# Kernel optimization log

Measured on AMD Instinct MI355X. Metric: run time of the kernel, lower is better.

## Reference

```python
import jax, jax.numpy as jnp
import numpy as np

N, M, E = 100000, 500, 300000
XS, GS, OUT, HEADS = 100, 100, 100, 2
SLOPE = 0.2
EPS = 1e-12


def l2norm(x, axis):
    n = jnp.linalg.norm(x, axis=axis, keepdims=True)
    return x / jnp.maximum(n, EPS)


def gat_layer(h_ijk, ends, n, W, att):
    # W: [heads*out, in_dim] (no bias); att: [1, heads, out]
    heads, out = att.shape[1], att.shape[2]
    c = (h_ijk @ W.T).reshape(-1, heads, out)               # [E, H, D]
    a = jnp.sum(att * c, axis=2, keepdims=True)             # [E, H, 1]
    e = jnp.exp(-jax.nn.leaky_relu(a, SLOPE))
    denom = jax.ops.segment_sum(e, ends, num_segments=n)    # [n, H, 1]
    alpha = e / denom[ends]                                 # segment softmax (dropout=eval/identity)
    h = jax.ops.segment_sum(alpha * c, ends, num_segments=n)  # [n, H, D]
    h = jax.nn.elu(h)
    h = l2norm(h, axis=2)
    return h.reshape(n, heads * out)


def merge_layer(h_in, h_out, Wi, bi, Wo, bo, Wl, bl):
    hi = h_in @ Wi.T + bi
    ho = h_out @ Wo.T + bo
    lam = jax.nn.sigmoid(jnp.concatenate([hi, ho], axis=1) @ Wl.T + bl)
    h = lam * hi + (1.0 - lam) * ho
    return l2norm(jax.nn.elu(h), axis=1)


def setup_inputs() -> dict:
    key = jax.random.key(0)
    ks = jax.random.split(key, 24)
    D = HEADS * OUT  # 200
    in1 = 2 * XS + GS   # 300
    in2 = 3 * D         # 600
    s = 0.05
    return {
        'edge_idx': jax.random.randint(ks[0], (2, E), 0, N),
        'edge_type': jax.random.randint(ks[1], (E,), 0, M),
        'path_idx': jax.random.randint(ks[2], (2, 8), 0, N),
        'path_type': jax.random.randint(ks[3], (2, 8), 0, M),
        'use_path': 0,
        'x': jax.random.normal(ks[4], (N, XS), jnp.float32),
        'g': jax.random.normal(ks[5], (M, GS), jnp.float32),
        'W_in1': s * jax.random.normal(ks[6], (D, in1), jnp.float32),
        'att_in1': s * jax.random.normal(ks[7], (1, HEADS, OUT), jnp.float32),
        'W_out1': s * jax.random.normal(ks[8], (D, in1), jnp.float32),
        'att_out1': s * jax.random.normal(ks[9], (1, HEADS, OUT), jnp.float32),
        'Wi1': s * jax.random.normal(ks[10], (D, D), jnp.float32), 'bi1': jnp.zeros((D,), jnp.float32),
        'Wo1': s * jax.random.normal(ks[11], (D, D), jnp.float32), 'bo1': jnp.zeros((D,), jnp.float32),
        'Wl1': s * jax.random.normal(ks[12], (1, 2 * D), jnp.float32), 'bl1': jnp.zeros((1,), jnp.float32),
        'Wr': s * jax.random.normal(ks[13], (D, GS), jnp.float32), 'br': jnp.zeros((D,), jnp.float32),
        'Wf': s * jax.random.normal(ks[14], (D, in1), jnp.float32), 'bf': jnp.zeros((D,), jnp.float32),
        'W_in2': s * jax.random.normal(ks[15], (D, in2), jnp.float32),
        'att_in2': s * jax.random.normal(ks[16], (1, 1, D), jnp.float32),
        'W_out2': s * jax.random.normal(ks[17], (D, in2), jnp.float32),
        'att_out2': s * jax.random.normal(ks[18], (1, 1, D), jnp.float32),
        'Wi2': s * jax.random.normal(ks[19], (D, D), jnp.float32), 'bi2': jnp.zeros((D,), jnp.float32),
        'Wo2': s * jax.random.normal(ks[20], (D, D), jnp.float32), 'bo2': jnp.zeros((D,), jnp.float32),
        'Wl2': s * jax.random.normal(ks[21], (1, 2 * D), jnp.float32), 'bl2': jnp.zeros((1,), jnp.float32),
        'W_ent': s * jax.random.normal(ks[22], (D, XS), jnp.float32),
    }


def reference(edge_idx, edge_type, path_idx, path_type, use_path, x, g,
              W_in1, att_in1, W_out1, att_out1, Wi1, bi1, Wo1, bo1, Wl1, bl1,
              Wr, br, Wf, bf,
              W_in2, att_in2, W_out2, att_out2, Wi2, bi2, Wo2, bo2, Wl2, bl2,
              W_ent):
    n, m = x.shape[0], g.shape[0]
    x = l2norm(x, axis=1)  # x_initial is renormalized each forward
    row, col = edge_idx[0], edge_idx[1]
    # hop 1: gather-concat per-edge features [E, 2*XS+GS]
    h_ijk = jnp.concatenate([x[row], x[col], g[edge_type]], axis=1)
    h_in = gat_layer(h_ijk, col, n, W_in1, att_in1)
    h_out = gat_layer(h_ijk, row, n, W_out1, att_out1)
    h = merge_layer(h_in, h_out, Wi1, bi1, Wo1, bo1, Wl1, bl1)
    # relation layer
    g_edges = jax.ops.segment_sum(h_ijk, edge_type, num_segments=m)
    g_edges = jax.nn.elu(l2norm(g_edges, axis=1))
    g_prime = (g @ Wr.T + br) + (g_edges @ Wf.T + bf)
    # hop 2
    h_ijk2 = jnp.concatenate([h[row], h[col], g_prime[edge_type]], axis=1)
    h_in2 = gat_layer(h_ijk2, col, n, W_in2, att_in2)
    h_out2 = gat_layer(h_ijk2, row, n, W_out2, att_out2)
    h = merge_layer(h_in2, h_out2, Wi2, bi2, Wo2, bo2, Wl2, bl2)
    # entity residual layer
    h_prime = x @ W_ent.T + h
    return h_prime
```

## Files before the change

### kernel.cpp

```cpp
#include <hip/hip_runtime.h>
#include <cstddef>
#include <cstdint>

#define WSLOPE 0.2f
#define WEPS 1e-12f

typedef __attribute__((ext_vector_type(8))) short bf16x8;
typedef __attribute__((ext_vector_type(4))) float f32x4;

__device__ __forceinline__ float waveSum(float v) {
#pragma unroll
    for (int off = 32; off > 0; off >>= 1) v += __shfl_xor(v, off, 64);
    return v;
}
__device__ __forceinline__ float rowSum16(float v) {
#pragma unroll
    for (int off = 8; off > 0; off >>= 1) v += __shfl_xor(v, off, 64);
    return v;
}
__device__ __forceinline__ float eluf(float v) { return v > 0.f ? v : expm1f(v); }
__device__ __forceinline__ short f2bf(float f) {
    union { float f; uint32_t u; } v; v.f = f;
    uint32_t r = v.u + 0x7FFF + ((v.u >> 16) & 1);
    return (short)(r >> 16);
}
__device__ __forceinline__ float bf2f(short s) {
    union { uint32_t u; float f; } v; v.u = ((uint32_t)(uint16_t)s) << 16;
    return v.f;
}

__global__ void k_invnorm(const float* __restrict__ x, float* __restrict__ invn, int N) {
    int wid = blockIdx.x * 4 + (threadIdx.x >> 6);
    int lane = threadIdx.x & 63;
    if (wid >= N) return;
    const float* p = x + (size_t)wid * 100;
    float a = p[lane];
    float ss = a * a;
    if (lane < 36) { float b = p[lane + 64]; ss += b * b; }
    ss = waveSum(ss);
    if (lane == 0) invn[wid] = 1.f / fmaxf(sqrtf(ss), WEPS);
}

__global__ void k_count(const int* __restrict__ keys, int* __restrict__ cnt, int n) {
    int i = blockIdx.x * 256 + threadIdx.x;
    if (i < n) atomicAdd(&cnt[keys[i]], 1);
}

#define SCAN_CHUNK 2048
__global__ void k_blocksum(const int* __restrict__ cnt, int* __restrict__ bsum, int n) {
    __shared__ int sh[256];
    int b = blockIdx.x, t = threadIdx.x;
    int base = b * SCAN_CHUNK;
    int s = 0;
    for (int i = t; i < SCAN_CHUNK; i += 256) { int idx = base + i; if (idx < n) s += cnt[idx]; }
    sh[t] = s; __syncthreads();
    for (int off = 128; off > 0; off >>= 1) { if (t < off) sh[t] += sh[t + off]; __syncthreads(); }
    if (t == 0) bsum[b] = sh[0];
}

__global__ void k_scanwrite(const int* __restrict__ cnt, const int* __restrict__ bsum,
                            int* __restrict__ offs, int* __restrict__ cur, int n, int nb) {
    __shared__ int sh[256];
    __shared__ int sbase;
    int b = blockIdx.x, t = threadIdx.x;
    if (t == 0) { int s = 0; for (int i = 0; i < b; ++i) s += bsum[i]; sbase = s; }
    __syncthreads();
    int base = b * SCAN_CHUNK;
    int loc[8]; int ts = 0;
#pragma unroll
    for (int i = 0; i < 8; ++i) { int idx = base + t * 8 + i; int v = (idx < n) ? cnt[idx] : 0; loc[i] = ts; ts += v; }
    sh[t] = ts; __syncthreads();
    for (int off = 1; off < 256; off <<= 1) {
        int v = (t >= off) ? sh[t - off] : 0;
// ... 15 lines not shown
                           const int* __restrict__ et, int* __restrict__ cur,
                           int* __restrict__ nbrS, int* __restrict__ etS,
                           int* __restrict__ keyS, int n) {
    int i = blockIdx.x * 256 + threadIdx.x;
    if (i < n) {
        int p = atomicAdd(&cur[keys[i]], 1);
        nbrS[p] = other[i];
        etS[p] = et[i];
        keyS[p] = keys[i];
    }
}

__global__ void k_scatter2(const int* __restrict__ keys, int* __restrict__ cur,
                           int* __restrict__ rs, int* __restrict__ cs,
                           const int* __restrict__ row, const int* __restrict__ col, int n) {
    int i = blockIdx.x * 256 + threadIdx.x;
    if (i < n) {
        int p = atomicAdd(&cur[keys[i]], 1);
        rs[p] = row[i];
        cs[p] = col[i];
    }
}

__global__ void k_watt(const float* __restrict__ att, const float* __restrict__ W,
                       float* __restrict__ wa, int H, int DH, int K) {
    int id = blockIdx.x * 256 + threadIdx.x;
    if (id >= H * K) return;
    int h = id / K, k = id % K;
    float s = 0.f;
    for (int j = 0; j < DH; ++j) s += att[h * DH + j] * W[(size_t)(h * DH + j) * K + k];
    wa[id] = s;
}

__global__ void k_dots2(const float* __restrict__ x, const float* __restrict__ invn,
                        const float* __restrict__ wai, const float* __restrict__ wao,
                        float* __restrict__ rdi, float* __restrict__ cdi,
                        float* __restrict__ rdo, float* __restrict__ cdo, int N) {
    int wid = blockIdx.x * 4 + (threadIdx.x >> 6);
    int lane = threadIdx.x & 63;
    if (wid >= N) return;
    float inv = invn[wid];
    const float* p = x + (size_t)wid * 100;
    float f0 = p[lane] * inv;
    float f1 = (lane < 36) ? p[lane + 64] * inv : 0.f;
#pragma unroll
    for (int h = 0; h < 2; ++h) {
        const float* wi = wai + h * 300;
        const float* wo = wao + h * 300;
        float ri = f0 * wi[lane] + ((lane < 36) ? f1 * wi[lane + 64] : 0.f);
        float ci = f0 * wi[100 + lane] + ((lane < 36) ? f1 * wi[100 + lane + 64] : 0.f);
        float ro = f0 * wo[lane] + ((lane < 36) ? f1 * wo[lane + 64] : 0.f);
        float co = f0 * wo[100 + lane] + ((lane < 36) ? f1 * wo[100 + lane + 64] : 0.f);
        ri = waveSum(ri); ci = waveSum(ci); ro = waveSum(ro); co = waveSum(co);
        if (lane == 0) { rdi[wid * 2 + h] = ri; cdi[wid * 2 + h] = ci; rdo[wid * 2 + h] = ro; cdo[wid * 2 + h] = co; }
    }
}

__global__ void k_gdot4(const float* __restrict__ g, const float* __restrict__ wai,
                        const float* __restrict__ wao, float* __restrict__ gdi,
                        float* __restrict__ gdo, int M) {
    int m = blockIdx.x * 256 + threadIdx.x;
    if (m >= M) return;
    const float* gm = g + (size_t)m * 100;
    float s0 = 0.f, s1 = 0.f, s2 = 0.f, s3 = 0.f;
    for (int k = 0; k < 100; ++k) {
        float v = gm[k];
        s0 += v * wai[200 + k]; s1 += v * wai[500 + k];
        s2 += v * wao[200 + k]; s3 += v * wao[500 + k];
    }
    gdi[m * 2] = s0; gdi[m * 2 + 1] = s1;
    gdo[m * 2] = s2; gdo[m * 2 + 1] = s3;
}

__global__ void k_ew_s(const int* __restrict__ nbrS, const int* __restrict__ keyS,
                       const int* __restrict__ etS,
                       const float* __restrict__ ndot, const float* __restrict__ kdot,
                       const float* __restrict__ gdot, float* __restrict__ ewS, int E, int H) {
    int id = blockIdx.x * 256 + threadIdx.x;
    if (id >= E * H) return;
    int p = id / H, h = id - p * H;
    float a = ndot[nbrS[p] * H + h] + kdot[keyS[p] * H + h] + gdot[etS[p] * H + h];
    float lr = a > 0.f ? a : WSLOPE * a;
    ewS[id] = expf(-lr);
}

template<bool HOP2>
__global__ void k_agg(const int* __restrict__ offs, const int* __restrict__ nbrS,
                      const int* __restrict__ etS, const float* __restrict__ ewS,
                      const short* __restrict__ featB, const short* __restrict__ gB,
                      short* __restrict__ A, int n0, int n1) {
    constexpr int H = HOP2 ? 1 : 2;
    constexpr int LDA = HOP2 ? 672 : 576;
    constexpr int FW = HOP2 ? 224 : 112;
    constexpr int GW = HOP2 ? 224 : 112;
    int node = n0 + blockIdx.x * 4 + (threadIdx.x >> 6);
    int lane = threadIdx.x & 63;
    if (node >= n1) return;
    int o = offs[node];
    int deg = offs[node + 1] - o;
    float va[7];
#pragma unroll
    for (int m = 0; m < 7; ++m) va[m] = 0.f;
    if (deg > 0) {
        float s0 = 0.f, s1 = 0.f;
        for (int i = lane; i < deg; i += 64) {
            s0 += ewS[(size_t)(o + i) * H];
            if (H == 2) s1 += ewS[(size_t)(o + i) * H + 1];
        }
        s0 = waveSum(s0);
        float rd0 = 1.f / s0, rd1 = rd0;
        if (H == 2) { s1 = waveSum(s1); rd1 = 1.f / s1; }
        for (int j = 0; j < deg; ++j) {
            float a0 = ewS[(size_t)(o + j) * H] * rd0;
            float a1 = (H == 2) ? ewS[(size_t)(o + j) * H + 1] * rd1 : a0;
            int nbr = nbrS[o + j];
            int et = etS[o + j];
// ... 22 lines not shown
    short* Ar = A + rb * LDA;
    if (!HOP2) {
#pragma unroll
        for (int m = 0; m < 7; ++m) {
            int d = lane + m * 64;
            if (d < 400) {
                int col = d < 100 ? d : (d < 200 ? d + 12 : (d < 300 ? d + 24 : d + 36));
                Ar[col] = f2bf(va[m]);
            }
        }
        if (lane < 48) { int q = lane / 12; int rm = lane - q * 12; Ar[q * 112 + 100 + rm] = 0; }
        const short* sf = featB + (size_t)node * 112;
#pragma unroll
        for (int mm = 0; mm < 2; ++mm) {
            int k = lane + mm * 64;
            if (k < 128) Ar[448 + k] = (deg > 0 && k < 112) ? sf[k] : (short)0;
        }
    } else {
#pragma unroll
        for (int m = 0; m < 7; ++m) {
            int d = lane + m * 64;
            if (d < 424) Ar[d < 200 ? d : d + 24] = f2bf(va[m]);
        }
        if (lane < 24) Ar[200 + lane] = 0;
        const short* sf = featB + (size_t)node * 224;
#pragma unroll
        for (int mm = 0; mm < 4; ++mm) {
            int k = lane + mm * 64;
            if (k < 224) Ar[448 + k] = deg > 0 ? sf[k] : (short)0;
        }
    }
}

template<int KSTEPS, bool BIAS, bool ACC>
__launch_bounds__(256)
__global__ void k_mgemm(const short* __restrict__ A, const short* __restrict__ Wb,
                        const float* __restrict__ bias,
                        float* __restrict__ out, int rows, int lda) {
    constexpr int LDW = KSTEPS * 32;
    const int t = threadIdx.x;
    const int wv = t >> 6, l = t & 63;
    const int lhi = l >> 4, llo = l & 15;
    const int rbase = blockIdx.x * 64 + wv * 16;
    f32x4 acc[13];
#pragma unroll
    for (int j = 0; j < 13; ++j) acc[j] = f32x4{0.f, 0.f, 0.f, 0.f};
    const short* arow = A + (size_t)(rbase + llo) * lda + lhi * 8;
#pragma unroll
    for (int kt = 0; kt < KSTEPS; ++kt) {
        bf16x8 a = *(const bf16x8*)(arow + kt * 32);
#pragma unroll
        for (int j = 0; j < 13; ++j) {
            bf16x8 b = *(const bf16x8*)(Wb + (size_t)(j * 16 + llo) * LDW + kt * 32 + lhi * 8);
            acc[j] = __builtin_amdgcn_mfma_f32_16x16x32_bf16(a, b, acc[j], 0, 0, 0);
        }
    }
    const int r0 = rbase + lhi * 4;
#pragma unroll
    for (int e = 0; e < 4; ++e) {
        int r = r0 + e;
        if (r >= rows) continue;
        float* orow = out + (size_t)r * 200;
#pragma unroll
        for (int j = 0; j < 13; ++j) {
            int d = j * 16 + llo;
            if (d < 200) {
                float v = acc[j][e];
                if (BIAS) v += bias[d];
                if (ACC) v += orow[d];
                orow[d] = v;
            }
        }
    }
}

template<int KSTEPS, int H>
__launch_bounds__(256)
__global__ void k_mgemm_post(const short* __restrict__ A, const short* __restrict__ Wb,
                             short* __restrict__ post, int rows, int lda) {
    constexpr int LDW = KSTEPS * 32;
    const int t = threadIdx.x;
    const int wv = t >> 6, l = t & 63;
    const int lhi = l >> 4, llo = l & 15;
    const int rbase = blockIdx.x * 64 + wv * 16;
    f32x4 acc[13];
#pragma unroll
    for (int j = 0; j < 13; ++j) acc[j] = f32x4{0.f, 0.f, 0.f, 0.f};
    const short* arow = A + (size_t)(rbase + llo) * lda + lhi * 8;
#pragma unroll
    for (int kt = 0; kt < KSTEPS; ++kt) {
        bf16x8 a = *(const bf16x8*)(arow + kt * 32);
#pragma unroll
        for (int j = 0; j < 13; ++j) {
            bf16x8 b = *(const bf16x8*)(Wb + (size_t)(j * 16 + llo) * LDW + kt * 32 + lhi * 8);
            acc[j] = __builtin_amdgcn_mfma_f32_16x16x32_bf16(a, b, acc[j], 0, 0, 0);
        }
    }
    const int r0 = rbase + lhi * 4;
#pragma unroll
    for (int e = 0; e < 4; ++e) {
        int r = r0 + e;
        if (r >= rows) continue;
        float v[13];
        float s0 = 0.f, s1 = 0.f;
#pragma unroll
        for (int j = 0; j < 13; ++j) {
            int d = j * 16 + llo;
            if (d < 200) {
                float xv = eluf(acc[j][e]);
                v[j] = xv;
                if (H == 1 || d < 100) s0 += xv * xv; else s1 += xv * xv;
            }
        }
        s0 = rowSum16(s0);
        float inv0 = 1.f / fmaxf(sqrtf(s0), WEPS);
        float inv1 = inv0;
        if (H == 2) { s1 = rowSum16(s1); inv1 = 1.f / fmaxf(sqrtf(s1), WEPS); }
        short* pr = post + (size_t)r * 224;
#pragma unroll
        for (int j = 0; j < 13; ++j) {
            int d = j * 16 + llo;
            if (d < 200) pr[d] = f2bf(v[j] * ((H == 2 && d >= 100) ? inv1 : inv0));
        }
    }
}

template<bool HOP1>
__launch_bounds__(256)
__global__ void k_mergemm(const short* __restrict__ pA, const short* __restrict__ pB,
                          const short* __restrict__ Wi, const short* __restrict__ Wo,
                          const float* __restrict__ bi, const float* __restrict__ bo,
                          const float* __restrict__ Wl, const float* __restrict__ bl,
                          float* __restrict__ outf, short* __restrict__ h1b,
                          const float* __restrict__ wa2i, const float* __restrict__ wa2o,
                          float* __restrict__ rdi, float* __restrict__ cdi,
                          float* __restrict__ rdo, float* __restrict__ cdo,
                          int rows) {
    const int t = threadIdx.x;
    const int wv = t >> 6, l = t & 63;
    const int lhi = l >> 4, llo = l & 15;
    const int rbase = blockIdx.x * 64 + wv * 16;
    f32x4 accA[13], accB[13];
#pragma unroll
    for (int j = 0; j < 13; ++j) { accA[j] = f32x4{0.f, 0.f, 0.f, 0.f}; accB[j] = f32x4{0.f, 0.f, 0.f, 0.f}; }
    const short* aA = pA + (size_t)(rbase + llo) * 224 + lhi * 8;
    const short* aB = pB + (size_t)(rbase + llo) * 224 + lhi * 8;
#pragma unroll
    for (int kt = 0; kt < 7; ++kt) {
        bf16x8 a1 = *(const bf16x8*)(aA + kt * 32);
        bf16x8 a2 = *(const bf16x8*)(aB + kt * 32);
#pragma unroll
        for (int j = 0; j < 13; ++j) {
            bf16x8 b1 = *(const bf16x8*)(Wi + (size_t)(j * 16 + llo) * 224 + kt * 32 + lhi * 8);
            accA[j] = __builtin_amdgcn_mfma_f32_16x16x32_bf16(a1, b1, accA[j], 0, 0, 0);
            bf16x8 b2 = *(const bf16x8*)(Wo + (size_t)(j * 16 + llo) * 224 + kt * 32 + lhi * 8);
            accB[j] = __builtin_amdgcn_mfma_f32_16x16x32_bf16(a2, b2, accB[j], 0, 0, 0);
        }
    }
    const int r0 = rbase + lhi * 4;
    float blv = bl[0];
#pragma unroll
    for (int e = 0; e < 4; ++e) {
        int r = r0 + e;
        if (r >= rows) continue;
        float vi[13], vo[13];
        float lp = 0.f;
#pragma unroll
        for (int j = 0; j < 13; ++j) {
            int d = j * 16 + llo;
            if (d < 200) {
                vi[j] = accA[j][e] + bi[d];
                vo[j] = accB[j][e] + bo[d];
                lp += Wl[d] * vi[j] + Wl[200 + d] * vo[j];
            }
        }
        lp = rowSum16(lp);
        float lam = 1.f / (1.f + expf(-(lp + blv)));
        float hv[13];
        float ss = 0.f;
#pragma unroll
        for (int j = 0; j < 13; ++j) {
            int d = j * 16 + llo;
            if (d < 200) { hv[j] = eluf(lam * vi[j] + (1.f - lam) * vo[j]); ss += hv[j] * hv[j]; }
        }
        ss = rowSum16(ss);
        float inv = 1.f / fmaxf(sqrtf(ss), WEPS);
        float ri = 0.f, ci = 0.f, ro = 0.f, co = 0.f;
#pragma unroll
        for (int j = 0; j < 13; ++j) {
            int d = j * 16 + llo;
            if (d < 200) {
                float val = hv[j] * inv;
                if (HOP1) {
                    h1b[(size_t)r * 224 + d] = f2bf(val);
                    ri += val * wa2i[d]; ci += val * wa2i[200 + d];
                    ro += val * wa2o[d]; co += val * wa2o[200 + d];
                } else {
                    outf[(size_t)r * 200 + d] = val;
                }
            } else if (HOP1) {
                h1b[(size_t)r * 224 + d] = 0;
            }
        }
        if (HOP1) {
            h1b[(size_t)r * 224 + 208 + llo] = 0;
            ri = rowSum16(ri); ci = rowSum16(ci); ro = rowSum16(ro); co = rowSum16(co);
            if (llo == 0) { rdi[r] = ri; cdi[r] = ci; rdo[r] = ro; cdo[r] = co; }
        }
    }
}

__launch_bounds__(256)
__global__ void k_mgemm_rel(const short* __restrict__ A, const short* __restrict__ Wb,
                            const float* __restrict__ brf,
                            short* __restrict__ gout, const float* __restrict__ wai,
                            const float* __restrict__ wao,
                            float* __restrict__ gdi, float* __restrict__ gdo, int rows) {
    constexpr int KSTEPS = 14, LDW = KSTEPS * 32;
    const int t = threadIdx.x;
    const int wv = t >> 6, l = t & 63;
    const int lhi = l >> 4, llo = l & 15;
    const int rbase = blockIdx.x * 64 + wv * 16;
    f32x4 acc[13];
#pragma unroll
    for (int j = 0; j < 13; ++j) acc[j] = f32x4{0.f, 0.f, 0.f, 0.f};
    const short* arow = A + (size_t)(rbase + llo) * 448 + lhi * 8;
#pragma unroll
    for (int kt = 0; kt < KSTEPS; ++kt) {
        bf16x8 a = *(const bf16x8*)(arow + kt * 32);
#pragma unroll
        for (int j = 0; j < 13; ++j) {
// ... 27 lines not shown
}

__global__ void k_prepw(const float* __restrict__ W, int ldW, int koff, int Klen, int span,
                        int mode, short* __restrict__ Wb, int ldWb, int dst) {
    int id = blockIdx.x * 256 + threadIdx.x;
    int tot = 208 * span;
    if (id >= tot) return;
    int d = id / span, k = id - d * span;
    float v = 0.f;
    if (d < 200) {
        if (mode == 0) { if (k < Klen) v = W[(size_t)d * ldW + koff + k]; }
        else { int h = d / 100; int kk = k - h * 112; if (kk >= 0 && kk < Klen) v = W[(size_t)d * ldW + koff + kk]; }
    }
    Wb[(size_t)d * ldWb + dst + k] = f2bf(v);
}

__global__ void k_prepwrf(const float* __restrict__ Wr, const float* __restrict__ Wf,
                          short* __restrict__ Wb) {
    int id = blockIdx.x * 256 + threadIdx.x;
    if (id >= 208 * 448) return;
    int d = id / 448, k = id - d * 448;
    float v = 0.f;
    if (d < 200) {
        if (k < 100) v = Wr[(size_t)d * 100 + k];
        else if (k >= 128 && k < 428) v = Wf[(size_t)d * 300 + (k - 128)];
    }
    Wb[id] = f2bf(v);
}

__global__ void k_brf(const float* __restrict__ br, const float* __restrict__ bf,
                      float* __restrict__ brf) {
    int d = threadIdx.x;
    if (d < 200) brf[d] = br[d] + bf[d];
}

__global__ void k_cvt112(const float* __restrict__ src, const float* __restrict__ invn,
                         short* __restrict__ dst, int rows) {
    int id = blockIdx.x * 256 + threadIdx.x;
    if (id >= rows * 112) return;
    int r = id / 112, k = id - r * 112;
    float v = 0.f;
    if (k < 100) { v = src[(size_t)r * 100 + k]; if (invn) v *= invn[r]; }
    dst[id] = f2bf(v);
}

__global__ void k_gcb(const float* __restrict__ g, short* __restrict__ gb, int rows) {
    int id = blockIdx.x * 256 + threadIdx.x;
    if (id >= rows * 128) return;
    int r = id >> 7, k = id & 127;
    gb[(size_t)r * 448 + k] = f2bf(k < 100 ? g[(size_t)r * 100 + k] : 0.f);
}

__global__ void k_gedges_b(const int* __restrict__ rsT, const int* __restrict__ csT,
                           const int* __restrict__ offsT,
                           const float* __restrict__ x, const float* __restrict__ invn,
                           const float* __restrict__ g, short* __restrict__ gcomb, int M) {
    __shared__ float red[6];
    int m = blockIdx.x, t = threadIdx.x;
    int o = offsT[m];
    int deg = offsT[m + 1] - o;
    float acc = 0.f;
    if (t < 128) {
        int d = t; bool ok = d < 100;
        for (int i = 0; i < deg; ++i) {
            int r = rsT[o + i];
            if (ok) acc += x[(size_t)r * 100 + d] * invn[r];
        }
    } else if (t < 256) {
        int d = t - 128; bool ok = d < 100;
        for (int i = 0; i < deg; ++i) {
            int c = csT[o + i];
            if (ok) acc += x[(size_t)c * 100 + d] * invn[c];
        }
    } else {
        int d = t - 256;
        if (d < 100) acc = (float)deg * g[(size_t)m * 100 + d];
    }
    float sq = waveSum(acc * acc);
    if ((t & 63) == 0) red[t >> 6] = sq;
    __syncthreads();
    float s2 = red[0] + red[1] + red[2] + red[3] + red[4] + red[5];
    float inv = 1.f / fmaxf(sqrtf(s2), WEPS);
    short* orow = gcomb + (size_t)m * 448 + 128;
// ... 63 lines not shown
    int* keyS_out= (int*)alloc((size_t)E * 4);
    int* rsT     = (int*)alloc((size_t)E * 4);
    int* csT     = (int*)alloc((size_t)E * 4);
    int* cnt     = (int*)alloc((size_t)N * 4);
    int* cur     = (int*)alloc((size_t)N * 4);
    int* bsum    = (int*)alloc((size_t)64 * 4);
    float* wa1_in = (float*)alloc((size_t)640 * 4);
    float* wa1_out= (float*)alloc((size_t)640 * 4);
    float* wa2_in = (float*)alloc((size_t)640 * 4);
    float* wa2_out= (float*)alloc((size_t)640 * 4);
    float* rdot_in = (float*)alloc((size_t)N * 2 * 4);
    float* cdot_in = (float*)alloc((size_t)N * 2 * 4);
    float* rdot_out= (float*)alloc((size_t)N * 2 * 4);
    float* cdot_out= (float*)alloc((size_t)N * 2 * 4);
    float* gdot_in = (float*)alloc((size_t)M * 2 * 4);
    float* gdot_out= (float*)alloc((size_t)M * 2 * 4);
    float* ewS_in  = (float*)alloc((size_t)E * 2 * 4);
    float* ewS_out = (float*)alloc((size_t)E * 2 * 4);
    short* gcomb   = (short*)alloc((size_t)Mr * 448 * 2);
    short* Wc_in1  = (short*)alloc((size_t)208 * 576 * 2);
    short* Wc_out1 = (short*)alloc((size_t)208 * 576 * 2);
    short* Wc_in2  = (short*)alloc((size_t)208 * 672 * 2);
    short* Wc_out2 = (short*)alloc((size_t)208 * 672 * 2);
    short* Wm_i1   = (short*)alloc((size_t)208 * 224 * 2);
    short* Wm_o1   = (short*)alloc((size_t)208 * 224 * 2);
    short* Wm_i2   = (short*)alloc((size_t)208 * 224 * 2);
    short* Wm_o2   = (short*)alloc((size_t)208 * 224 * 2);
    short* Wb_ent  = (short*)alloc((size_t)208 * 128 * 2);
    short* Wrf_b   = (short*)alloc((size_t)208 * 448 * 2);
    float* brf     = (float*)alloc((size_t)200 * 4);

    if (off_b >= ws_size) return;
    size_t rem = ws_size - off_b;
    long long Cll = (long long)(rem / 2368);
    long long Nr64 = ((long long)N + 63) & ~63LL;
    int C = (int)(Cll > Nr64 ? Nr64 : Cll);
    C &= ~63;
    if (C < 64) return;
    short* Ac    = (short*)alloc((size_t)C * 672 * 2);
    short* postA = (short*)alloc((size_t)C * 224 * 2);
    short* postB = (short*)alloc((size_t)C * 224 * 2);
    if (off_b > ws_size) return;

    const int gE = (E + 255) / 256;
    const int gN4 = (N + 3) / 4;
    const int gM64 = (M + 63) / 64;

    k_invnorm<<<gN4, 256, 0, stream>>>(x, invn, N);

    hipMemsetAsync(postA, 0, (size_t)C * 224 * 2, stream);
    hipMemsetAsync(postB, 0, (size_t)C * 224 * 2, stream);

    k_cvt112<<<((int)(((size_t)N * 112 + 255) / 256)), 256, 0, stream>>>(x, invn, xn_bf, N);
    k_cvt112<<<((int)(((size_t)M * 112 + 255) / 256)), 256, 0, stream>>>(g, nullptr, g_bf, M);

    auto gsp = [](int span) { return (208 * span + 255) / 256; };
    k_prepw<<<gsp(224), 256, 0, stream>>>(W_in1, 300, 0, 100, 224, 1, Wc_in1, 576, 0);
    k_prepw<<<gsp(224), 256, 0, stream>>>(W_in1, 300, 200, 100, 224, 1, Wc_in1, 576, 224);
    k_prepw<<<gsp(128), 256, 0, stream>>>(W_in1, 300, 100, 100, 128, 0, Wc_in1, 576, 448);
    k_prepw<<<gsp(224), 256, 0, stream>>>(W_out1, 300, 100, 100, 224, 1, Wc_out1, 576, 0);
    k_prepw<<<gsp(224), 256, 0, stream>>>(W_out1, 300, 200, 100, 224, 1, Wc_out1, 576, 224);
    k_prepw<<<gsp(128), 256, 0, stream>>>(W_out1, 300, 0, 100, 128, 0, Wc_out1, 576, 448);
    k_prepw<<<gsp(224), 256, 0, stream>>>(W_in2, 600, 0, 200, 224, 0, Wc_in2, 672, 0);
    k_prepw<<<gsp(224), 256, 0, stream>>>(W_in2, 600, 400, 200, 224, 0, Wc_in2, 672, 224);
    k_prepw<<<gsp(224), 256, 0, stream>>>(W_in2, 600, 200, 200, 224, 0, Wc_in2, 672, 448);
    k_prepw<<<gsp(224), 256, 0, stream>>>(W_out2, 600, 200, 200, 224, 0, Wc_out2, 672, 0);
    k_prepw<<<gsp(224), 256, 0, stream>>>(W_out2, 600, 400, 200, 224, 0, Wc_out2, 672, 224);
    k_prepw<<<gsp(224), 256, 0, stream>>>(W_out2, 600, 0, 200, 224, 0, Wc_out2, 672, 448);
    k_prepw<<<gsp(224), 256, 0, stream>>>(Wi1, 200, 0, 200, 224, 0, Wm_i1, 224, 0);
    k_prepw<<<gsp(224), 256, 0, stream>>>(Wo1, 200, 0, 200, 224, 0, Wm_o1, 224, 0);
    k_prepw<<<gsp(224), 256, 0, stream>>>(Wi2, 200, 0, 200, 224, 0, Wm_i2, 224, 0);
    k_prepw<<<gsp(224), 256, 0, stream>>>(Wo2, 200, 0, 200, 224, 0, Wm_o2, 224, 0);
    k_prepw<<<gsp(128), 256, 0, stream>>>(W_ent, 100, 0, 100, 128, 0, Wb_ent, 128, 0);
    k_prepwrf<<<gsp(448), 256, 0, stream>>>(Wr, Wf, Wrf_b);
    k_brf<<<1, 256, 0, stream>>>(br, bf, brf);

    int nbN = (N + SCAN_CHUNK - 1) / SCAN_CHUNK;
    int nbM = (M + SCAN_CHUNK - 1) / SCAN_CHUNK;
    hipMemsetAsync(cnt, 0, (size_t)N * 4, stream);
    k_count<<<gE, 256, 0, stream>>>(col, cnt, E);
    k_blocksum<<<nbN, 256, 0, stream>>>(cnt, bsum, N);
    k_scanwrite<<<nbN, 256, 0, stream>>>(cnt, bsum, offs_in, cur, N, nbN);
    k_scatter3<<<gE, 256, 0, stream>>>(col, row, etype, cur, nbrS_in, etS_in, keyS_in, E);

    hipMemsetAsync(cnt, 0, (size_t)N * 4, stream);
    k_count<<<gE, 256, 0, stream>>>(row, cnt, E);
    k_blocksum<<<nbN, 256, 0, stream>>>(cnt, bsum, N);
    k_scanwrite<<<nbN, 256, 0, stream>>>(cnt, bsum, offs_out, cur, N, nbN);
    k_scatter3<<<gE, 256, 0, stream>>>(row, col, etype, cur, nbrS_out, etS_out, keyS_out, E);

    hipMemsetAsync(cnt, 0, (size_t)M * 4, stream);
    k_count<<<gE, 256, 0, stream>>>(etype, cnt, E);
    k_blocksum<<<nbM, 256, 0, stream>>>(cnt, bsum, M);
    k_scanwrite<<<nbM, 256, 0, stream>>>(cnt, bsum, offsT, cur, M, nbM);
    k_scatter2<<<gE, 256, 0, stream>>>(etype, cur, rsT, csT, row, col, E);

    k_watt<<<(600 + 255) / 256, 256, 0, stream>>>(att_in1, W_in1, wa1_in, 2, 100, 300);
    k_watt<<<(600 + 255) / 256, 256, 0, stream>>>(att_out1, W_out1, wa1_out, 2, 100, 300);
    k_watt<<<(600 + 255) / 256, 256, 0, stream>>>(att_in2, W_in2, wa2_in, 1, 200, 600);
    k_watt<<<(600 + 255) / 256, 256, 0, stream>>>(att_out2, W_out2, wa2_out, 1, 200, 600);

    k_dots2<<<gN4, 256, 0, stream>>>(x, invn, wa1_in, wa1_out, rdot_in, cdot_in, rdot_out, cdot_out, N);
    k_gdot4<<<(M + 255) / 256, 256, 0, stream>>>(g, wa1_in, wa1_out, gdot_in, gdot_out, M);
    k_ew_s<<<(E * 2 + 255) / 256, 256, 0, stream>>>(nbrS_in, keyS_in, etS_in, rdot_in, cdot_in, gdot_in, ewS_in, E, 2);
    k_ew_s<<<(E * 2 + 255) / 256, 256, 0, stream>>>(nbrS_out, keyS_out, etS_out, cdot_out, rdot_out, gdot_out, ewS_out, E, 2);
    k_gcb<<<((int)(((size_t)M * 128 + 255) / 256)), 256, 0, stream>>>(g, gcomb, M);

    for (int n0 = 0; n0 < N; n0 += C) {
        int rows = (N - n0 < C) ? (N - n0) : C;
        int n1 = n0 + rows;
        int ga = (rows + 3) / 4;
        int gb = (rows + 63) / 64;
        k_agg<false><<<ga, 256, 0, stream>>>(offs_in, nbrS_in, etS_in, ewS_in, xn_bf, g_bf, Ac, n0, n1);
        k_mgemm_post<18, 2><<<gb, 256, 0, stream>>>(Ac, Wc_in1, postA, rows, 576);
        k_agg<false><<<ga, 256, 0, stream>>>(offs_out, nbrS_out, etS_out, ewS_out, xn_bf, g_bf, Ac, n0, n1);
        k_mgemm_post<18, 2><<<gb, 256, 0, stream>>>(Ac, Wc_out1, postB, rows, 576);
        k_mergemm<true><<<gb, 256, 0, stream>>>(postA, postB, Wm_i1, Wm_o1, bi1, bo1, Wl1, bl1,
                                                nullptr, h1_bf + (size_t)n0 * 224, wa2_in, wa2_out,
                                                rdot_in + n0, cdot_in + n0, rdot_out + n0, cdot_out + n0,
                                                rows);
    }

    k_gedges_b<<<M, 384, 0, stream>>>(rsT, csT, offsT, x, invn, g, gcomb, M);
    k_mgemm_rel<<<gM64, 256, 0, stream>>>(gcomb, Wrf_b, brf, gp_bf, wa2_in, wa2_out, gdot_in, gdot_out, M);

    k_ew_s<<<(E + 255) / 256, 256, 0, stream>>>(nbrS_in, keyS_in, etS_in, rdot_in, cdot_in, gdot_in, ewS_in, E, 1);
    k_ew_s<<<(E + 255) / 256, 256, 0, stream>>>(nbrS_out, keyS_out, etS_out, cdot_out, rdot_out, gdot_out, ewS_out, E, 1);

    for (int n0 = 0; n0 < N; n0 += C) {
        int rows = (N - n0 < C) ? (N - n0) : C;
        int n1 = n0 + rows;
        int ga = (rows + 3) / 4;
        int gb = (rows + 63) / 64;
        k_agg<true><<<ga, 256, 0, stream>>>(offs_in, nbrS_in, etS_in, ewS_in, h1_bf, gp_bf, Ac, n0, n1);
        k_mgemm_post<21, 1><<<gb, 256, 0, stream>>>(Ac, Wc_in2, postA, rows, 672);
        k_agg<true><<<ga, 256, 0, stream>>>(offs_out, nbrS_out, etS_out, ewS_out, h1_bf, gp_bf, Ac, n0, n1);
        k_mgemm_post<21, 1><<<gb, 256, 0, stream>>>(Ac, Wc_out2, postB, rows, 672);
        k_mergemm<false><<<gb, 256, 0, stream>>>(postA, postB, Wm_i2, Wm_o2, bi2, bo2, Wl2, bl2,
                                                 out + (size_t)n0 * 200, nullptr, nullptr, nullptr,
                                                 nullptr, nullptr, nullptr, nullptr, rows);
        k_mgemm<4, false, true><<<gb, 256, 0, stream>>>(xn_bf + (size_t)n0 * 112, Wb_ent, nullptr,
                                                        out + (size_t)n0 * 200, rows, 112);
    }
}
```

Measured before the change: 2.859 ms.

## Fuse GAT projection, merge and entity residual GEMMs into one kernel via LDS

Merges the per-direction projection GEMM with ELU/L2 post-processing, the merge-layer GEMMs, and the entity residual GEMM into a single kernel. The normalized per-direction outputs stay in shared memory instead of round-tripping through global postA/postB buffers. Node and relation preprocessing (norm, bf16 conversion, attention dots) are also fused into single kernels, and the in/out edge-weight kernels become one launch. The cost is two aggregation buffers per chunk instead of one, which shrinks the chunk size, plus higher LDS and register use in the fused kernel.

```diff
diff --git a/kernel.cpp b/kernel.cpp
--- a/kernel.cpp
+++ b/kernel.cpp
@@ -29,16 +29,65 @@
     return v.f;
 }
 
-__global__ void k_invnorm(const float* __restrict__ x, float* __restrict__ invn, int N) {
+__global__ void k_nodeprep(const float* __restrict__ x, float* __restrict__ invn,
+                           short* __restrict__ xnb,
+                           const float* __restrict__ wai, const float* __restrict__ wao,
+                           float* __restrict__ rdi, float* __restrict__ cdi,
+                           float* __restrict__ rdo, float* __restrict__ cdo, int N) {
     int wid = blockIdx.x * 4 + (threadIdx.x >> 6);
     int lane = threadIdx.x & 63;
     if (wid >= N) return;
     const float* p = x + (size_t)wid * 100;
-    float a = p[lane];
-    float ss = a * a;
-    if (lane < 36) { float b = p[lane + 64]; ss += b * b; }
-    ss = waveSum(ss);
-    if (lane == 0) invn[wid] = 1.f / fmaxf(sqrtf(ss), WEPS);
+    float a0 = p[lane];
+    float a1 = (lane < 36) ? p[lane + 64] : 0.f;
+    float ss = waveSum(a0 * a0 + a1 * a1);
+    float inv = 1.f / fmaxf(sqrtf(ss), WEPS);
+    if (lane == 0) invn[wid] = inv;
+    float f0 = a0 * inv, f1 = a1 * inv;
+    short* xb = xnb + (size_t)wid * 112;
+    xb[lane] = f2bf(f0);
+    if (lane < 36) xb[64 + lane] = f2bf(f1);
+    else if (lane < 48) xb[64 + lane] = 0;
+#pragma unroll
+    for (int h = 0; h < 2; ++h) {
+        const float* wi = wai + h * 300;
+        const float* wo = wao + h * 300;
+        float ri = f0 * wi[lane] + f1 * wi[lane + 64];
+        float ci = f0 * wi[100 + lane] + f1 * wi[100 + lane + 64];
+        float ro = f0 * wo[lane] + f1 * wo[lane + 64];
+        float co = f0 * wo[100 + lane] + f1 * wo[100 + lane + 64];
+        ri = waveSum(ri); ci = waveSum(ci); ro = waveSum(ro); co = waveSum(co);
+        if (lane == 0) { rdi[wid * 2 + h] = ri; cdi[wid * 2 + h] = ci; rdo[wid * 2 + h] = ro; cdo[wid * 2 + h] = co; }
+    }
+}
+
+__global__ void k_gprep(const float* __restrict__ g, short* __restrict__ gbf,
+                        short* __restrict__ gcomb,
+                        const float* __restrict__ wai, const float* __restrict__ wao,
+                        float* __restrict__ gdi, float* __restrict__ gdo, int M) {
+    int m = blockIdx.x * 4 + (threadIdx.x >> 6);
+    int lane = threadIdx.x & 63;
+    if (m >= M) return;
+    const float* gm = g + (size_t)m * 100;
+    float v0 = gm[lane];
+    float v1 = (lane < 36) ? gm[lane + 64] : 0.f;
+    short b0 = f2bf(v0), b1 = (lane < 36) ? f2bf(v1) : (short)0;
+    short* gb = gbf + (size_t)m * 112;
+    gb[lane] = b0;
+    if (lane < 48) gb[64 + lane] = (lane < 36) ? b1 : (short)0;
+    short* gc = gcomb + (size_t)m * 448;
+    gc[lane] = b0;
+    gc[64 + lane] = b1;
+    float s0 = v0 * wai[200 + lane];
+    float s1 = v0 * wai[500 + lane];
+    float s2 = v0 * wao[200 + lane];
+    float s3 = v0 * wao[500 + lane];
+    if (lane < 36) {
+        s0 += v1 * wai[264 + lane]; s1 += v1 * wai[564 + lane];
+        s2 += v1 * wao[264 + lane]; s3 += v1 * wao[564 + lane];
+    }
+    s0 = waveSum(s0); s1 = waveSum(s1); s2 = waveSum(s2); s3 = waveSum(s3);
+    if (lane == 0) { gdi[m * 2] = s0; gdi[m * 2 + 1] = s1; gdo[m * 2] = s2; gdo[m * 2 + 1] = s3; }
 }
 
 __global__ void k_count(const int* __restrict__ keys, int* __restrict__ cnt, int n) {
@@ -120,56 +169,29 @@
     wa[id] = s;
 }
 
-__global__ void k_dots2(const float* __restrict__ x, const float* __restrict__ invn,
-                        const float* __restrict__ wai, const float* __restrict__ wao,
-                        float* __restrict__ rdi, float* __restrict__ cdi,
-                        float* __restrict__ rdo, float* __restrict__ cdo, int N) {
-    int wid = blockIdx.x * 4 + (threadIdx.x >> 6);
-    int lane = threadIdx.x & 63;
-    if (wid >= N) return;
-    float inv = invn[wid];
-    const float* p = x + (size_t)wid * 100;
-    float f0 = p[lane] * inv;
-    float f1 = (lane < 36) ? p[lane + 64] * inv : 0.f;
-#pragma unroll
-    for (int h = 0; h < 2; ++h) {
-        const float* wi = wai + h * 300;
-        const float* wo = wao + h * 300;
-        float ri = f0 * wi[lane] + ((lane < 36) ? f1 * wi[lane + 64] : 0.f);
-        float ci = f0 * wi[100 + lane] + ((lane < 36) ? f1 * wi[100 + lane + 64] : 0.f);
-        float ro = f0 * wo[lane] + ((lane < 36) ? f1 * wo[lane + 64] : 0.f);
-        float co = f0 * wo[100 + lane] + ((lane < 36) ? f1 * wo[100 + lane + 64] : 0.f);
-        ri = waveSum(ri); ci = waveSum(ci); ro = waveSum(ro); co = waveSum(co);
-        if (lane == 0) { rdi[wid * 2 + h] = ri; cdi[wid * 2 + h] = ci; rdo[wid * 2 + h] = ro; cdo[wid * 2 + h] = co; }
-    }
-}
-
-__global__ void k_gdot4(const float* __restrict__ g, const float* __restrict__ wai,
-                        const float* __restrict__ wao, float* __restrict__ gdi,
-                        float* __restrict__ gdo, int M) {
-    int m = blockIdx.x * 256 + threadIdx.x;
-    if (m >= M) return;
-    const float* gm = g + (size_t)m * 100;
-    float s0 = 0.f, s1 = 0.f, s2 = 0.f, s3 = 0.f;
-    for (int k = 0; k < 100; ++k) {
-        float v = gm[k];
-        s0 += v * wai[200 + k]; s1 += v * wai[500 + k];
-        s2 += v * wao[200 + k]; s3 += v * wao[500 + k];
-    }
-    gdi[m * 2] = s0; gdi[m * 2 + 1] = s1;
-    gdo[m * 2] = s2; gdo[m * 2 + 1] = s3;
-}
-
-__global__ void k_ew_s(const int* __restrict__ nbrS, const int* __restrict__ keyS,
-                       const int* __restrict__ etS,
-                       const float* __restrict__ ndot, const float* __restrict__ kdot,
-                       const float* __restrict__ gdot, float* __restrict__ ewS, int E, int H) {
+__global__ void k_ew2(const int* __restrict__ nbi, const int* __restrict__ kyi,
+                      const int* __restrict__ eti,
+                      const int* __restrict__ nbo, const int* __restrict__ kyo,
+                      const int* __restrict__ eto,
+                      const float* __restrict__ rdi, const float* __restrict__ cdi,
+                      const float* __restrict__ rdo, const float* __restrict__ cdo,
+                      const float* __restrict__ gdi, const float* __restrict__ gdo,
+                      float* __restrict__ ewi, float* __restrict__ ewo, int E, int H) {
     int id = blockIdx.x * 256 + threadIdx.x;
-    if (id >= E * H) return;
-    int p = id / H, h = id - p * H;
-    float a = ndot[nbrS[p] * H + h] + kdot[keyS[p] * H + h] + gdot[etS[p] * H + h];
-    float lr = a > 0.f ? a : WSLOPE * a;
-    ewS[id] = expf(-lr);
+    int tot = E * H;
+    if (id >= 2 * tot) return;
+    if (id < tot) {
+        int p = id / H, h = id - p * H;
+        float a = rdi[nbi[p] * H + h] + cdi[kyi[p] * H + h] + gdi[eti[p] * H + h];
+        float lr = a > 0.f ? a : WSLOPE * a;
+        ewi[id] = expf(-lr);
+    } else {
+        int id2 = id - tot;
+        int p = id2 / H, h = id2 - p * H;
+        float a = cdo[nbo[p] * H + h] + rdo[kyo[p] * H + h] + gdo[eto[p] * H + h];
+        float lr = a > 0.f ? a : WSLOPE * a;
+        ewo[id2] = expf(-lr);
+    }
 }
 
 template<bool HOP2>
@@ -258,123 +280,81 @@
     }
 }
 
-template<int KSTEPS, bool BIAS, bool ACC>
+template<int KSTEPS, int H, bool HOP1>
 __launch_bounds__(256)
-__global__ void k_mgemm(const short* __restrict__ A, const short* __restrict__ Wb,
-                        const float* __restrict__ bias,
-                        float* __restrict__ out, int rows, int lda) {
-    constexpr int LDW = KSTEPS * 32;
+__global__ void k_gatmerge(const short* __restrict__ Ain, const short* __restrict__ Aout,
+                           const short* __restrict__ WcA, const short* __restrict__ WcB,
+                           const short* __restrict__ Wi, const short* __restrict__ Wo,
+                           const float* __restrict__ bi, const float* __restrict__ bo,
+                           const float* __restrict__ Wl, const float* __restrict__ bl,
+                           const short* __restrict__ xnb, const short* __restrict__ Went,
+                           float* __restrict__ outf, short* __restrict__ h1b,
+                           const float* __restrict__ wa2i, const float* __restrict__ wa2o,
+                           float* __restrict__ rdi, float* __restrict__ cdi,
+                           float* __restrict__ rdo, float* __restrict__ cdo,
+                           int rows) {
+    constexpr int LDA = KSTEPS * 32;
+    __shared__ short pL[2][64][232];
     const int t = threadIdx.x;
     const int wv = t >> 6, l = t & 63;
     const int lhi = l >> 4, llo = l & 15;
     const int rbase = blockIdx.x * 64 + wv * 16;
-    f32x4 acc[13];
-#pragma unroll
-    for (int j = 0; j < 13; ++j) acc[j] = f32x4{0.f, 0.f, 0.f, 0.f};
-    const short* arow = A + (size_t)(rbase + llo) * lda + lhi * 8;
-#pragma unroll
-    for (int kt = 0; kt < KSTEPS; ++kt) {
-        bf16x8 a = *(const bf16x8*)(arow + kt * 32);
-#pragma unroll
-        for (int j = 0; j < 13; ++j) {
-            bf16x8 b = *(const bf16x8*)(Wb + (size_t)(j * 16 + llo) * LDW + kt * 32 + lhi * 8);
-            acc[j] = __builtin_amdgcn_mfma_f32_16x16x32_bf16(a, b, acc[j], 0, 0, 0);
-        }
-    }
-    const int r0 = rbase + lhi * 4;
-#pragma unroll
-    for (int e = 0; e < 4; ++e) {
-        int r = r0 + e;
-        if (r >= rows) continue;
-        float* orow = out + (size_t)r * 200;
-#pragma unroll
-        for (int j = 0; j < 13; ++j) {
-            int d = j * 16 + llo;
-            if (d < 200) {
-                float v = acc[j][e];
-                if (BIAS) v += bias[d];
-                if (ACC) v += orow[d];
-                orow[d] = v;
-            }
-        }
-    }
-}
-
-template<int KSTEPS, int H>
-__launch_bounds__(256)
-__global__ void k_mgemm_post(const short* __restrict__ A, const short* __restrict__ Wb,
-                             short* __restrict__ post, int rows, int lda) {
-    constexpr int LDW = KSTEPS * 32;
-    const int t = threadIdx.x;
-    const int wv = t >> 6, l = t & 63;
-    const int lhi = l >> 4, llo = l & 15;
-    const int rbase = blockIdx.x * 64 + wv * 16;
-    f32x4 acc[13];
-#pragma unroll
-    for (int j = 0; j < 13; ++j) acc[j] = f32x4{0.f, 0.f, 0.f, 0.f};
-    const short* arow = A + (size_t)(rbase + llo) * lda + lhi * 8;
-#pragma unroll
-    for (int kt = 0; kt < KSTEPS; ++kt) {
-        bf16x8 a = *(const bf16x8*)(arow + kt * 32);
-#pragma unroll
-        for (int j = 0; j < 13; ++j) {
-            bf16x8 b = *(const bf16x8*)(Wb + (size_t)(j * 16 + llo) * LDW + kt * 32 + lhi * 8);
-            acc[j] = __builtin_amdgcn_mfma_f32_16x16x32_bf16(a, b, acc[j], 0, 0, 0);
-        }
-    }
-    const int r0 = rbase + lhi * 4;
-#pragma unroll
-    for (int e = 0; e < 4; ++e) {
-        int r = r0 + e;
-        if (r >= rows) continue;
-        float v[13];
-        float s0 = 0.f, s1 = 0.f;
-#pragma unroll
-        for (int j = 0; j < 13; ++j) {
-            int d = j * 16 + llo;
-            if (d < 200) {
-                float xv = eluf(acc[j][e]);
-                v[j] = xv;
-                if (H == 1 || d < 100) s0 += xv * xv; else s1 += xv * xv;
-            }
-        }
-        s0 = rowSum16(s0);
-        float inv0 = 1.f / fmaxf(sqrtf(s0), WEPS);
-        float inv1 = inv0;
-        if (H == 2) { s1 = rowSum16(s1); inv1 = 1.f / fmaxf(sqrtf(s1), WEPS); }
-        short* pr = post + (size_t)r * 224;
-#pragma unroll
-        for (int j = 0; j < 13; ++j) {
-            int d = j * 16 + llo;
-            if (d < 200) pr[d] = f2bf(v[j] * ((H == 2 && d >= 100) ? inv1 : inv0));
-        }
-    }
-}
-
-template<bool HOP1>
-__launch_bounds__(256)
-__global__ void k_mergemm(const short* __restrict__ pA, const short* __restrict__ pB,
-                          const short* __restrict__ Wi, const short* __restrict__ Wo,
-                          const float* __restrict__ bi, const float* __restrict__ bo,
-                          const float* __restrict__ Wl, const float* __restrict__ bl,
-                          float* __restrict__ outf, short* __restrict__ h1b,
-                          const float* __restrict__ wa2i, const float* __restrict__ wa2o,
-                          float* __restrict__ rdi, float* __restrict__ cdi,
-                          float* __restrict__ rdo, float* __restrict__ cdo,
-                          int rows) {
-    const int t = threadIdx.x;
-    const int wv = t >> 6, l = t & 63;
-    const int lhi = l >> 4, llo = l & 15;
-    const int rbase = blockIdx.x * 64 + wv * 16;
+
+#pragma unroll 1
+    for (int dir = 0; dir < 2; ++dir) {
+        const short* A = dir ? Aout : Ain;
+        const short* Wc = dir ? WcB : WcA;
+        f32x4 acc[13];
+#pragma unroll
+        for (int j = 0; j < 13; ++j) acc[j] = f32x4{0.f, 0.f, 0.f, 0.f};
+        const short* arow = A + (size_t)(rbase + llo) * LDA + lhi * 8;
+#pragma unroll
+        for (int kt = 0; kt < KSTEPS; ++kt) {
+            bf16x8 a = *(const bf16x8*)(arow + kt * 32);
+#pragma unroll
+            for (int j = 0; j < 13; ++j) {
+                bf16x8 b = *(const bf16x8*)(Wc + (size_t)(j * 16 + llo) * LDA + kt * 32 + lhi * 8);
+                acc[j] = __builtin_amdgcn_mfma_f32_16x16x32_bf16(a, b, acc[j], 0, 0, 0);
+            }
+        }
+#pragma unroll
+        for (int e = 0; e < 4; ++e) {
+            float v[13];
+            float s0 = 0.f, s1 = 0.f;
+#pragma unroll
+            for (int j = 0; j < 13; ++j) {
+                int d = j * 16 + llo;
+                if (d < 200) {
+                    float xv = eluf(acc[j][e]);
+                    v[j] = xv;
+                    if (H == 1 || d < 100) s0 += xv * xv; else s1 += xv * xv;
+                }
+            }
+            s0 = rowSum16(s0);
+            float inv0 = 1.f / fmaxf(sqrtf(s0), WEPS);
+            float inv1 = inv0;
+            if (H == 2) { s1 = rowSum16(s1); inv1 = 1.f / fmaxf(sqrtf(s1), WEPS); }
+            short* pr = &pL[dir][wv * 16 + lhi * 4 + e][0];
+#pragma unroll
+            for (int j = 0; j < 13; ++j) {
+                int d = j * 16 + llo;
+                if (d < 200) pr[d] = f2bf(v[j] * ((H == 2 && d >= 100) ? inv1 : inv0));
+                else pr[d] = 0;
+            }
+            pr[208 + llo] = 0;
+        }
+    }
+    __syncthreads();
+
     f32x4 accA[13], accB[13];
 #pragma unroll
     for (int j = 0; j < 13; ++j) { accA[j] = f32x4{0.f, 0.f, 0.f, 0.f}; accB[j] = f32x4{0.f, 0.f, 0.f, 0.f}; }
-    const short* aA = pA + (size_t)(rbase + llo) * 224 + lhi * 8;
-    const short* aB = pB + (size_t)(rbase + llo) * 224 + lhi * 8;
+    const short* pa = &pL[0][wv * 16 + llo][0];
+    const short* pb = &pL[1][wv * 16 + llo][0];
 #pragma unroll
     for (int kt = 0; kt < 7; ++kt) {
-        bf16x8 a1 = *(const bf16x8*)(aA + kt * 32);
-        bf16x8 a2 = *(const bf16x8*)(aB + kt * 32);
+        bf16x8 a1 = *(const bf16x8*)(pa + kt * 32 + lhi * 8);
+        bf16x8 a2 = *(const bf16x8*)(pb + kt * 32 + lhi * 8);
 #pragma unroll
         for (int j = 0; j < 13; ++j) {
             bf16x8 b1 = *(const bf16x8*)(Wi + (size_t)(j * 16 + llo) * 224 + kt * 32 + lhi * 8);
@@ -383,6 +363,22 @@
             accB[j] = __builtin_amdgcn_mfma_f32_16x16x32_bf16(a2, b2, accB[j], 0, 0, 0);
         }
     }
+    f32x4 accR[13];
+    if (!HOP1) {
+#pragma unroll
+        for (int j = 0; j < 13; ++j) accR[j] = f32x4{0.f, 0.f, 0.f, 0.f};
+        const short* xr = xnb + (size_t)(rbase + llo) * 112 + lhi * 8;
+#pragma unroll
+        for (int kt = 0; kt < 4; ++kt) {
+            bf16x8 a = *(const bf16x8*)(xr + kt * 32);
+#pragma unroll
+            for (int j = 0; j < 13; ++j) {
+                bf16x8 b = *(const bf16x8*)(Went + (size_t)(j * 16 + llo) * 128 + kt * 32 + lhi * 8);
+                accR[j] = __builtin_amdgcn_mfma_f32_16x16x32_bf16(a, b, accR[j], 0, 0, 0);
+            }
+        }
+    }
+
     const int r0 = rbase + lhi * 4;
     float blv = bl[0];
 #pragma unroll
@@ -422,7 +418,7 @@
                     ri += val * wa2i[d]; ci += val * wa2i[200 + d];
                     ro += val * wa2o[d]; co += val * wa2o[200 + d];
                 } else {
-                    outf[(size_t)r * 200 + d] = val;
+                    outf[(size_t)r * 200 + d] = val + accR[j][e];
                 }
             } else if (HOP1) {
                 h1b[(size_t)r * 224 + d] = 0;
@@ -516,23 +512,6 @@
                       float* __restrict__ brf) {
     int d = threadIdx.x;
     if (d < 200) brf[d] = br[d] + bf[d];
-}
-
-__global__ void k_cvt112(const float* __restrict__ src, const float* __restrict__ invn,
-                         short* __restrict__ dst, int rows) {
-    int id = blockIdx.x * 256 + threadIdx.x;
-    if (id >= rows * 112) return;
-    int r = id / 112, k = id - r * 112;
-    float v = 0.f;
-    if (k < 100) { v = src[(size_t)r * 100 + k]; if (invn) v *= invn[r]; }
-    dst[id] = f2bf(v);
-}
-
-__global__ void k_gcb(const float* __restrict__ g, short* __restrict__ gb, int rows) {
-    int id = blockIdx.x * 256 + threadIdx.x;
-    if (id >= rows * 128) return;
-    int r = id >> 7, k = id & 127;
-    gb[(size_t)r * 448 + k] = f2bf(k < 100 ? g[(size_t)r * 100 + k] : 0.f);
 }
 
 __global__ void k_gedges_b(const int* __restrict__ rsT, const int* __restrict__ csT,
@@ -662,27 +641,19 @@
 
     if (off_b >= ws_size) return;
     size_t rem = ws_size - off_b;
-    long long Cll = (long long)(rem / 2368);
+    long long Cll = (long long)(rem / 2816);
     long long Nr64 = ((long long)N + 63) & ~63LL;
     int C = (int)(Cll > Nr64 ? Nr64 : Cll);
     C &= ~63;
     if (C < 64) return;
-    short* Ac    = (short*)alloc((size_t)C * 672 * 2);
-    short* postA = (short*)alloc((size_t)C * 224 * 2);
-    short* postB = (short*)alloc((size_t)C * 224 * 2);
+    short* Ac0 = (short*)alloc((size_t)C * 672 * 2);
+    short* Ac1 = (short*)alloc((size_t)C * 672 * 2);
     if (off_b > ws_size) return;
 
     const int gE = (E + 255) / 256;
     const int gN4 = (N + 3) / 4;
+    const int gM4 = (M + 3) / 4;
     const int gM64 = (M + 63) / 64;
-
-    k_invnorm<<<gN4, 256, 0, stream>>>(x, invn, N);
-
-    hipMemsetAsync(postA, 0, (size_t)C * 224 * 2, stream);
-    hipMemsetAsync(postB, 0, (size_t)C * 224 * 2, stream);
-
-    k_cvt112<<<((int)(((size_t)N * 112 + 255) / 256)), 256, 0, stream>>>(x, invn, xn_bf, N);
-    k_cvt112<<<((int)(((size_t)M * 112 + 255) / 256)), 256, 0, stream>>>(g, nullptr, g_bf, M);
 
     auto gsp = [](int span) { return (208 * span + 255) / 256; };
     k_prepw<<<gsp(224), 256, 0, stream>>>(W_in1, 300, 0, 100, 224, 1, Wc_in1, 576, 0);
@@ -730,46 +701,49 @@
     k_watt<<<(600 + 255) / 256, 256, 0, stream>>>(att_in2, W_in2, wa2_in, 1, 200, 600);
     k_watt<<<(600 + 255) / 256, 256, 0, stream>>>(att_out2, W_out2, wa2_out, 1, 200, 600);
 
-    k_dots2<<<gN4, 256, 0, stream>>>(x, invn, wa1_in, wa1_out, rdot_in, cdot_in, rdot_out, cdot_out, N);
-    k_gdot4<<<(M + 255) / 256, 256, 0, stream>>>(g, wa1_in, wa1_out, gdot_in, gdot_out, M);
-    k_ew_s<<<(E * 2 + 255) / 256, 256, 0, stream>>>(nbrS_in, keyS_in, etS_in, rdot_in, cdot_in, gdot_in, ewS_in, E, 2);
-    k_ew_s<<<(E * 2 + 255) / 256, 256, 0, stream>>>(nbrS_out, keyS_out, etS_out, cdot_out, rdot_out, gdot_out, ewS_out, E, 2);
-    k_gcb<<<((int)(((size_t)M * 128 + 255) / 256)), 256, 0, stream>>>(g, gcomb, M);
+    k_nodeprep<<<gN4, 256, 0, stream>>>(x, invn, xn_bf, wa1_in, wa1_out,
+                                        rdot_in, cdot_in, rdot_out, cdot_out, N);
+    k_gprep<<<gM4, 256, 0, stream>>>(g, g_bf, gcomb, wa1_in, wa1_out, gdot_in, gdot_out, M);
+    k_ew2<<<(2 * E * 2 + 255) / 256, 256, 0, stream>>>(nbrS_in, keyS_in, etS_in,
+                                                       nbrS_out, keyS_out, etS_out,
+                                                       rdot_in, cdot_in, rdot_out, cdot_out,
+                                                       gdot_in, gdot_out, ewS_in, ewS_out, E, 2);
 
     for (int n0 = 0; n0 < N; n0 += C) {
         int rows = (N - n0 < C) ? (N - n0) : C;
         int n1 = n0 + rows;
         int ga = (rows + 3) / 4;
         int gb = (rows + 63) / 64;
-        k_agg<false><<<ga, 256, 0, stream>>>(offs_in, nbrS_in, etS_in, ewS_in, xn_bf, g_bf, Ac, n0, n1);
-        k_mgemm_post<18, 2><<<gb, 256, 0, stream>>>(Ac, Wc_in1, postA, rows, 576);
-        k_agg<false><<<ga, 256, 0, stream>>>(offs_out, nbrS_out, etS_out, ewS_out, xn_bf, g_bf, Ac, n0, n1);
-        k_mgemm_post<18, 2><<<gb, 256, 0, stream>>>(Ac, Wc_out1, postB, rows, 576);
-        k_mergemm<true><<<gb, 256, 0, stream>>>(postA, postB, Wm_i1, Wm_o1, bi1, bo1, Wl1, bl1,
-                                                nullptr, h1_bf + (size_t)n0 * 224, wa2_in, wa2_out,
-                                                rdot_in + n0, cdot_in + n0, rdot_out + n0, cdot_out + n0,
-                                                rows);
+        k_agg<false><<<ga, 256, 0, stream>>>(offs_in, nbrS_in, etS_in, ewS_in, xn_bf, g_bf, Ac0, n0, n1);
+        k_agg<false><<<ga, 256, 0, stream>>>(offs_out, nbrS_out, etS_out, ewS_out, xn_bf, g_bf, Ac1, n0, n1);
+        k_gatmerge<18, 2, true><<<gb, 256, 0, stream>>>(Ac0, Ac1, Wc_in1, Wc_out1, Wm_i1, Wm_o1,
+                                                        bi1, bo1, Wl1, bl1, nullptr, nullptr,
+                                                        nullptr, h1_bf + (size_t)n0 * 224,
+                                                        wa2_in, wa2_out,
+                                                        rdot_in + n0, cdot_in + n0,
+                                                        rdot_out + n0, cdot_out + n0, rows);
     }
 
     k_gedges_b<<<M, 384, 0, stream>>>(rsT, csT, offsT, x, invn, g, gcomb, M);
     k_mgemm_rel<<<gM64, 256, 0, stream>>>(gcomb, Wrf_b, brf, gp_bf, wa2_in, wa2_out, gdot_in, gdot_out, M);
 
-    k_ew_s<<<(E + 255) / 256, 256, 0, stream>>>(nbrS_in, keyS_in, etS_in, rdot_in, cdot_in, gdot_in, ewS_in, E, 1);
-    k_ew_s<<<(E + 255) / 256, 256, 0, stream>>>(nbrS_out, keyS_out, etS_out, cdot_out, rdot_out, gdot_out, ewS_out, E, 1);
+    k_ew2<<<(2 * E + 255) / 256, 256, 0, stream>>>(nbrS_in, keyS_in, etS_in,
+                                                   nbrS_out, keyS_out, etS_out,
+                                                   rdot_in, cdot_in, rdot_out, cdot_out,
+                                                   gdot_in, gdot_out, ewS_in, ewS_out, E, 1);
 
     for (int n0 = 0; n0 < N; n0 += C) {
         int rows = (N - n0 < C) ? (N - n0) : C;
         int n1 = n0 + rows;
         int ga = (rows + 3) / 4;
         int gb = (rows + 63) / 64;
-        k_agg<true><<<ga, 256, 0, stream>>>(offs_in, nbrS_in, etS_in, ewS_in, h1_bf, gp_bf, Ac, n0, n1);
-        k_mgemm_post<21, 1><<<gb, 256, 0, stream>>>(Ac, Wc_in2, postA, rows, 672);
-        k_agg<true><<<ga, 256, 0, stream>>>(offs_out, nbrS_out, etS_out, ewS_out, h1_bf, gp_bf, Ac, n0, n1);
-        k_mgemm_post<21, 1><<<gb, 256, 0, stream>>>(Ac, Wc_out2, postB, rows, 672);
-        k_mergemm<false><<<gb, 256, 0, stream>>>(postA, postB, Wm_i2, Wm_o2, bi2, bo2, Wl2, bl2,
-                                                 out + (size_t)n0 * 200, nullptr, nullptr, nullptr,
-                                                 nullptr, nullptr, nullptr, nullptr, rows);
-        k_mgemm<4, false, true><<<gb, 256, 0, stream>>>(xn_bf + (size_t)n0 * 112, Wb_ent, nullptr,
-                                                        out + (size_t)n0 * 200, rows, 112);
-    }
-}
+        k_agg<true><<<ga, 256, 0, stream>>>(offs_in, nbrS_in, etS_in, ewS_in, h1_bf, gp_bf, Ac0, n0, n1);
+        k_agg<true><<<ga, 256, 0, stream>>>(offs_out, nbrS_out, etS_out, ewS_out, h1_bf, gp_bf, Ac1, n0, n1);
+        k_gatmerge<21, 1, false><<<gb, 256, 0, stream>>>(Ac0, Ac1, Wc_in2, Wc_out2, Wm_i2, Wm_o2,
+                                                         bi2, bo2, Wl2, bl2,
+                                                         xn_bf + (size_t)n0 * 112, Wb_ent,
+                                                         out + (size_t)n0 * 200, nullptr,
+                                                         nullptr, nullptr,
+                                                         nullptr, nullptr, nullptr, nullptr, rows);
+    }
+}
```

Measured after the change: 3.079 ms. 1.08x slower.
